# Optimization experiments

Measured on AMD Instinct MI355X. Metric: run time of the kernel, lower is better.

The kernel has to match this reference:

```python
import jax, jax.numpy as jnp
import numpy as np
import math

B, T, C = 2, 2048, 2048
N_HEAD = 16
N_KV = 4
GROUP = N_HEAD // N_KV
HS = C // N_HEAD
WINDOW = 1024
SINK = 4


def setup_inputs() -> dict:
    key = jax.random.key(0)
    ks = jax.random.split(key, 5)
    s = 1.0 / math.sqrt(C)
    return {
        "x": jax.random.normal(ks[0], (B, T, C), dtype=jnp.float32),
        "Wq": jax.random.normal(ks[1], (C, C), dtype=jnp.float32) * s,
        "Wk": jax.random.normal(ks[2], (N_KV * HS, C), dtype=jnp.float32) * s,
        "Wv": jax.random.normal(ks[3], (N_KV * HS, C), dtype=jnp.float32) * s,
        "Wo": jax.random.normal(ks[4], (C, C), dtype=jnp.float32) * s,
    }


def _sliding_window_sink_mask(t):
    i = jnp.arange(t)[:, None]  # query index
    j = jnp.arange(t)[None, :]  # key index
    causal = j <= i
    band = j >= i - (WINDOW - 1)
    mask = causal & band
    mask = mask | (j < SINK)          # sink columns always visible
    mask = mask & ((i >= SINK) | causal)  # sink rows stay strictly causal
    return mask  # (T, T) bool


def reference(x, Wq, Wk, Wv, Wo):
    b, t, c = x.shape
    q = (x @ Wq.T).reshape(b, t, N_HEAD, HS).transpose(0, 2, 1, 3)
    # group q heads by kv head: (B, n_kv, group, T, hs)
    q = q.reshape(b, N_KV, GROUP, t, HS)
    k = (x @ Wk.T).reshape(b, t, N_KV, HS).transpose(0, 2, 1, 3)  # (B, n_kv, T, hs)
    v = (x @ Wv.T).reshape(b, t, N_KV, HS).transpose(0, 2, 1, 3)
    scale = 1.0 / math.sqrt(HS)
    # scores over full TxT (faithful to original, K/V expansion done via broadcast)
    att = jnp.einsum('bkgqd,bkjd->bkgqj', q, k) * scale
    mask = _sliding_window_sink_mask(t)  # (T, T)
    att = jnp.where(mask[None, None, None, :, :], att, -jnp.inf)
    att = jax.nn.softmax(att, axis=-1)
    y = jnp.einsum('bkgqj,bkjd->bkgqd', att, v)
    y = y.reshape(b, N_HEAD, t, HS).transpose(0, 2, 1, 3).reshape(b, t, c)
    return y @ Wo.T
```

## Files before the change

### kernel.cpp

```cpp
#include <hip/hip_runtime.h>


#define T_SEQ 2048
#define NKV   4
#define HS    128
#define CDIM  2048
#define QKVN  3072
#define WIN   1024
#define SINKN 4

typedef __bf16 bf16x8 __attribute__((ext_vector_type(8)));
typedef float  f32x4  __attribute__((ext_vector_type(4)));

#define MFMA16(A, B, C) __builtin_amdgcn_mfma_f32_16x16x32_bf16(A, B, C, 0, 0, 0)
#define EXP2(x) __builtin_amdgcn_exp2f(x)

__device__ inline unsigned short f2bu(float f) {
  unsigned int u = __float_as_uint(f);
  u += 0x7fffu + ((u >> 16) & 1u);
  return (unsigned short)(u >> 16);
}
__device__ inline unsigned int pkhi(float f0, float f1) {
  return __builtin_amdgcn_perm(__float_as_uint(f1), __float_as_uint(f0),
                               0x07060302u);
}
__device__ inline __bf16 us2b(unsigned short u) {
  union { unsigned short u; __bf16 b; } t; t.u = u; return t.b;
}
__device__ inline f32x4 fzero4() { f32x4 z = {0.f, 0.f, 0.f, 0.f}; return z; }

__device__ __forceinline__ void glds16(const void* g, const void* lds_uniform) {
  typedef __attribute__((address_space(1))) void gv;
  typedef __attribute__((address_space(3))) void lv;
  __builtin_amdgcn_global_load_lds((gv*)(unsigned long long)g,
                                   (lv*)(unsigned int)(unsigned long long)lds_uniform,
                                   16, 0, 0);
}

#define SZ_X  8388608
#define SZ_WQ 4194304
#define SZ_WK 1048576
#define OFF_WQ (SZ_X)
#define OFF_WK (SZ_X + SZ_WQ)
#define OFF_WV (OFF_WK + SZ_WK)
#define OFF_WO (OFF_WV + SZ_WK)
#define SZ_ALL (OFF_WO + SZ_WQ)

__global__ __launch_bounds__(256) void f2b_all(const float* __restrict__ x,
                                               const float* __restrict__ wq,
                                               const float* __restrict__ wk,
                                               const float* __restrict__ wv,
                                               const float* __restrict__ wo,
                                               unsigned short* __restrict__ out,
                                               float qs) {
  int i = (blockIdx.x * 256 + threadIdx.x) * 4;
  const float* src; int off; float sc = 1.0f;
  if (i < OFF_WQ)      { src = x;  off = 0; }
  else if (i < OFF_WK) { src = wq; off = OFF_WQ; sc = qs; }
  else if (i < OFF_WV) { src = wk; off = OFF_WK; }
  else if (i < OFF_WO) { src = wv; off = OFF_WV; }
  else                 { src = wo; off = OFF_WO; }
  float4 v = *reinterpret_cast<const float4*>(src + (i - off));
  ushort4 o;
  o.x = f2bu(v.x * sc); o.y = f2bu(v.y * sc);
  o.z = f2bu(v.z * sc); o.w = f2bu(v.w * sc);
  *reinterpret_cast<ushort4*>(out + i) = o;
}

__device__ inline void storeC(unsigned short* p, float v) { *p = f2bu(v); }
__device__ inline void storeC(float* p, float v) { *p = v; }

template <typename OutT>
__global__ __launch_bounds__(512, 2) void gemm_bn192(const unsigned short* __restrict__ A,
                                                     const unsigned short* __restrict__ B,
                                                     OutT* __restrict__ C,
                                                     int M, int N, int K) {
  __shared__ __align__(16) unsigned short As[2][16384];
  __shared__ __align__(16) unsigned short Bs[2][12288];
  const int tid  = threadIdx.x;
  const int wave = tid >> 6, lane = tid & 63;
  const int quad = lane >> 4, l16 = lane & 15;
  const int wmi  = wave >> 1, wni = wave & 1;
  const int sx   = ((l16 >> 3) & 1) << 5;

  const int tmn  = M >> 8;
  const int qq   = gridDim.x >> 3;
  const int swzb = (blockIdx.x & 7) * qq + (blockIdx.x >> 3);
  const int tm   = (swzb % tmn) << 8;
  const int tn   = (swzb / tmn) * 192;

  const int logl = (lane * 16) ^ (((lane >> 5) & 1) << 5);
  const int srow = logl >> 6;
  const int scol = (logl & 63) >> 1;
  const int NT   = K >> 6;

  auto issueA = [&](int tt, int ch) {
    glds16(&A[(size_t)(tm + (ch & 15) * 16 + srow) * K + (tt << 6) + (ch >> 4) * 32 + scol],
           (const char*)As + ((tt & 1) << 15) + ch * 1024);
  };
  auto issueB = [&](int tt, int kh, int rb) {
    glds16(&B[(size_t)(tn + rb * 16 + srow) * K + (tt << 6) + kh * 32 + scol],
           (const char*)Bs + (tt & 1) * 24576 + (kh * 12 + rb) * 1024);
  };
  const int g3kh = (wave >= 4) ? 1 : 0;
  const int g3rb = (wave >= 4) ? (wave - 4) : (8 + wave);

  f32x4 acc[4][6];
#pragma unroll
  for (int i = 0; i < 4; ++i)
#pragma unroll
    for (int j = 0; j < 6; ++j) acc[i][j] = fzero4();

  issueA(0, wave); issueA(0, 8 + wave); issueB(0, 0, wave);
  issueA(0, 16 + wave); issueA(0, 24 + wave); issueB(0, 1, 4 + wave);
  issueB(0, g3kh, g3rb);
  if (NT > 1) {
    issueA(1, wave); issueA(1, 8 + wave); issueB(1, 0, wave);
    asm volatile("s_waitcnt vmcnt(3)" ::: "memory");
  } else {
    asm volatile("s_waitcnt vmcnt(0)" ::: "memory");
  }
  __builtin_amdgcn_s_barrier();

  for (int t = 0; t < NT; ++t) {
    const char* Asc = (const char*)As + ((t & 1) << 15);
    const char* Bsc = (const char*)Bs + (t & 1) * 24576;
    const bool h1 = (t + 1 < NT), h2 = (t + 2 < NT);
    bf16x8 aq[4], bq[6];

#pragma unroll
    for (int g = 0; g < 6; ++g)
      bq[g] = *reinterpret_cast<const bf16x8*>(
          Bsc + (((wni * 96 + g * 16 + l16) << 6) + ((quad * 16) ^ sx)));
#pragma unroll
    for (int f = 0; f < 4; ++f)
      aq[f] = *reinterpret_cast<const bf16x8*>(
          Asc + (((wmi * 64 + f * 16 + l16) << 6) + ((quad * 16) ^ sx)));
    if (h1) {
      issueA(t + 1, 16 + wave); issueA(t + 1, 24 + wave);
      issueB(t + 1, 1, 4 + wave); issueB(t + 1, g3kh, g3rb);
    }
    __builtin_amdgcn_s_barrier();
    asm volatile("s_waitcnt lgkmcnt(0)" ::: "memory");
    __builtin_amdgcn_s_setprio(1);
#pragma unroll
    for (int f = 0; f < 4; ++f)
#pragma unroll
      for (int g = 0; g < 6; ++g) acc[f][g] = MFMA16(aq[f], bq[g], acc[f][g]);
    __builtin_amdgcn_s_setprio(0);
    if (h1) asm volatile("s_waitcnt vmcnt(7)" ::: "memory");
    else    asm volatile("s_waitcnt vmcnt(0)" ::: "memory");
    __builtin_amdgcn_s_barrier();

#pragma unroll
    for (int g = 0; g < 6; ++g)
      bq[g] = *reinterpret_cast<const bf16x8*>(
          Bsc + (12288 + ((wni * 96 + g * 16 + l16) << 6) + ((quad * 16) ^ sx)));
#pragma unroll
    for (int f = 0; f < 4; ++f)
      aq[f] = *reinterpret_cast<const bf16x8*>(
          Asc + (16384 + ((wmi * 64 + f * 16 + l16) << 6) + ((quad * 16) ^ sx)));
    if (h2) {
      issueA(t + 2, wave); issueA(t + 2, 8 + wave); issueB(t + 2, 0, wave);
    }
    __builtin_amdgcn_s_barrier();
    asm volatile("s_waitcnt lgkmcnt(0)" ::: "memory");
    __builtin_amdgcn_s_setprio(1);
#pragma unroll
    for (int f = 0; f < 4; ++f)
#pragma unroll
      for (int g = 0; g < 6; ++g) acc[f][g] = MFMA16(aq[f], bq[g], acc[f][g]);
    __builtin_amdgcn_s_setprio(0);
    if (h2)      asm volatile("s_waitcnt vmcnt(7)" ::: "memory");
    else if (h1) asm volatile("s_waitcnt vmcnt(4)" ::: "memory");
    else         asm volatile("s_waitcnt vmcnt(0)" ::: "memory");
    __builtin_amdgcn_s_barrier();
  }

#pragma unroll
  for (int fi = 0; fi < 4; ++fi)
#pragma unroll
    for (int g = 0; g < 6; ++g)
#pragma unroll
      for (int r = 0; r < 4; ++r) {
        const int row = tm + wmi * 64 + fi * 16 + quad * 4 + r;
        const int col = tn + wni * 96 + g * 16 + l16;
        storeC(&C[(size_t)row * N + col], acc[fi][g][r]);
      }
}

template <typename OutT>
__global__ __launch_bounds__(512, 2) void gemm_bn128(const unsigned short* __restrict__ A,
                                                     const unsigned short* __restrict__ B,
                                                     OutT* __restrict__ C,
                                                     int M, int N, int K) {
  __shared__ __align__(16) unsigned short As[2][16384];
  __shared__ __align__(16) unsigned short Bs[2][8192];
  const int tid  = threadIdx.x;
  const int wave = tid >> 6, lane = tid & 63;
  const int quad = lane >> 4, l16 = lane & 15;
  const int wmi  = wave >> 1, wni = wave & 1;
  const int sx   = ((l16 >> 3) & 1) << 5;

  const int tmn  = M >> 8;
  const int qq   = gridDim.x >> 3;
  const int swzb = (blockIdx.x & 7) * qq + (blockIdx.x >> 3);
  const int tm   = (swzb % tmn) << 8;
  const int tn   = (swzb / tmn) << 7;

  const int logl = (lane * 16) ^ (((lane >> 5) & 1) << 5);
  const int srow = logl >> 6;
  const int scol = (logl & 63) >> 1;
  const int NT   = K >> 6;

  auto issueA = [&](int tt, int ch) {
    glds16(&A[(size_t)(tm + (ch & 15) * 16 + srow) * K + (tt << 6) + (ch >> 4) * 32 + scol],
           (const char*)As + ((tt & 1) << 15) + ch * 1024);
  };
  auto issueB = [&](int tt, int ch) {
    glds16(&B[(size_t)(tn + (ch & 7) * 16 + srow) * K + (tt << 6) + (ch >> 3) * 32 + scol],
           (const char*)Bs + ((tt & 1) << 14) + ch * 1024);
  };

  f32x4 acc[4][4];
#pragma unroll
  for (int i = 0; i < 4; ++i)
#pragma unroll
    for (int j = 0; j < 4; ++j) acc[i][j] = fzero4();

  issueB(0, wave);     issueA(0, wave);      issueA(0, 8 + wave);
  issueB(0, 8 + wave); issueA(0, 16 + wave); issueA(0, 24 + wave);
  if (NT > 1) {
    issueB(1, wave); issueA(1, wave); issueA(1, 8 + wave);
    asm volatile("s_waitcnt vmcnt(6)" ::: "memory");
  } else {
    asm volatile("s_waitcnt vmcnt(3)" ::: "memory");
  }
  __builtin_amdgcn_s_barrier();

  for (int t = 0; t < NT; ++t) {
    const char* Asc = (const char*)As + ((t & 1) << 15);
    const char* Bsc = (const char*)Bs + ((t & 1) << 14);
    const bool h1 = (t + 1 < NT), h2 = (t + 2 < NT);
    bf16x8 aq[4], bq[4];

#pragma unroll
    for (int g = 0; g < 4; ++g)
      bq[g] = *reinterpret_cast<const bf16x8*>(
          Bsc + (((wni * 64 + g * 16 + l16) << 6) + ((quad * 16) ^ sx)));
#pragma unroll
    for (int f = 0; f < 4; ++f)
      aq[f] = *reinterpret_cast<const bf16x8*>(
          Asc + (((wmi * 64 + f * 16 + l16) << 6) + ((quad * 16) ^ sx)));
    if (h1) {
      issueB(t + 1, 8 + wave); issueA(t + 1, 16 + wave); issueA(t + 1, 24 + wave);
    }
    __builtin_amdgcn_s_barrier();
    asm volatile("s_waitcnt lgkmcnt(0)" ::: "memory");
    __builtin_amdgcn_s_setprio(1);
#pragma unroll
    for (int f = 0; f < 4; ++f)
#pragma unroll
      for (int g = 0; g < 4; ++g) acc[f][g] = MFMA16(aq[f], bq[g], acc[f][g]);
    __builtin_amdgcn_s_setprio(0);
    if (h1) asm volatile("s_waitcnt vmcnt(6)" ::: "memory");
    else    asm volatile("s_waitcnt vmcnt(0)" ::: "memory");
    __builtin_amdgcn_s_barrier();

#pragma unroll
    for (int g = 0; g < 4; ++g)
      bq[g] = *reinterpret_cast<const bf16x8*>(
          Bsc + (8192 + ((wni * 64 + g * 16 + l16) << 6) + ((quad * 16) ^ sx)));
#pragma unroll
    for (int f = 0; f < 4; ++f)
      aq[f] = *reinterpret_cast<const bf16x8*>(
          Asc + (16384 + ((wmi * 64 + f * 16 + l16) << 6) + ((quad * 16) ^ sx)));
    if (h2) {
      issueB(t + 2, wave); issueA(t + 2, wave); issueA(t + 2, 8 + wave);
    }
    __builtin_amdgcn_s_barrier();
    asm volatile("s_waitcnt lgkmcnt(0)" ::: "memory");
    __builtin_amdgcn_s_setprio(1);
#pragma unroll
    for (int f = 0; f < 4; ++f)
#pragma unroll
      for (int g = 0; g < 4; ++g) acc[f][g] = MFMA16(aq[f], bq[g], acc[f][g]);
    __builtin_amdgcn_s_setprio(0);
    if (h2)      asm volatile("s_waitcnt vmcnt(6)" ::: "memory");
    else if (h1) asm volatile("s_waitcnt vmcnt(3)" ::: "memory");
    else         asm volatile("s_waitcnt vmcnt(0)" ::: "memory");
    __builtin_amdgcn_s_barrier();
  }

#pragma unroll
  for (int fi = 0; fi < 4; ++fi)
#pragma unroll
    for (int g = 0; g < 4; ++g)
#pragma unroll
      for (int r = 0; r < 4; ++r) {
        const int row = tm + wmi * 64 + fi * 16 + quad * 4 + r;
        const int col = tn + wni * 64 + g * 16 + l16;
        storeC(&C[(size_t)row * N + col], acc[fi][g][r]);
      }
}

__global__ __launch_bounds__(256) void kvpack(const unsigned short* __restrict__ QKV,
                                              unsigned short* __restrict__ Kp,
                                              unsigned short* __restrict__ Vp) {
  const int tid  = threadIdx.x;
  const int kt64 = blockIdx.x;
  const int bk   = blockIdx.y;
  const int b = bk >> 2, kvh = bk & 3;
  const int kt = kt64 * 64;
  const int bT = b * T_SEQ;
  const int dq = tid & 15;

  unsigned short* kdst = &Kp[(size_t)(bk * 32 + kt64) * 8192];
#pragma unroll
  for (int it = 0; it < 4; ++it) {
    int key = it * 16 + (tid >> 4);
    float4 v = *reinterpret_cast<const float4*>(
        &QKV[(size_t)(bT + kt + key) * QKVN + 2048 + kvh * HS + dq * 8]);
    int c = dq >> 2, quad = dq & 3, nt = key & 3, l16s = key >> 2;
    *reinterpret_cast<float4*>(
        &kdst[((size_t)((c * 4 + nt) * 64 + quad * 16 + l16s)) * 8]) = v;
  }

#pragma unroll
  for (int it = 0; it < 4; ++it) {
    int key = it * 16 + (tid >> 4);
    float4 v = *reinterpret_cast<const float4*>(
        &QKV[(size_t)(bT + kt + key) * QKVN + 2560 + kvh * HS + dq * 8]);
    const unsigned short* pv = reinterpret_cast<const unsigned short*>(&v);
    int kt32 = kt64 * 2 + (key >> 5);
    int quad = (key & 31) >> 3, j = key & 7;
    unsigned short* vdst = &Vp[(size_t)(bk * 64 + kt32) * 4096];
#pragma unroll
    for (int j2 = 0; j2 < 8; ++j2) {
      int d = dq * 8 + j2, dt = d >> 4, l16v = d & 15;
      vdst[((size_t)(dt * 64 + quad * 16 + l16v)) * 8 + j] = pv[j2];
    }
  }
}

__global__ __launch_bounds__(256) void attn_kernel(const unsigned short* __restrict__ QKV,
                                                   const unsigned short* __restrict__ Kp,
                                                   const unsigned short* __restrict__ Vp,
                                                   unsigned short* __restrict__ Y) {
  __shared__ __align__(16) unsigned short Ks[2][8192];
  __shared__ __align__(16) unsigned short Vs[2][8192];
  __shared__ __align__(16) unsigned short Ps[4 * 2048];

  const int tid  = threadIdx.x;
  const int wave = tid >> 6, lane = tid & 63;
  const int quad = lane >> 4, l16 = lane & 15;
  const int bk   = blockIdx.x & 7;
  const int seq  = blockIdx.x >> 3;
  const int qt0  = (63 - seq) * 32;
  const int kvh  = bk & 3, b = bk >> 2;
  const int h    = kvh * 4 + wave;
  const int bT   = b * T_SEQ;
  char* Pw = (char*)&Ps[wave * 2048];

  bf16x8 qa[2][4];
#pragma unroll
  for (int mt = 0; mt < 2; ++mt)
#pragma unroll
    for (int c = 0; c < 4; ++c)
      qa[mt][c] = *reinterpret_cast<const bf16x8*>(
          &QKV[(size_t)(bT + qt0 + mt * 16 + l16) * QKVN + h * HS + c * 32 + quad * 8]);

  bf16x8 ones;
#pragma unroll
  for (int j = 0; j < 8; ++j) ones[j] = us2b(0x3F80);

  f32x4 o[2][9];
#pragma unroll
  for (int mt = 0; mt < 2; ++mt)
#pragma unroll
    for (int dt = 0; dt < 9; ++dt) o[mt][dt] = fzero4();

  const int start = (qt0 >= 1024) ? ((qt0 - 1023) & ~63) : 0;
  const int sink  = (start > 0) ? 1 : 0;
  const int nch   = ((qt0 + 32 - start + 63) >> 6) + sink;

  auto stage = [&](int ci, int buf) {
    const int kt = (sink && ci == 0) ? 0 : start + (ci - sink) * 64;
    const unsigned short* kg = &Kp[(size_t)(bk * 32 + (kt >> 6)) * 8192 + lane * 8];
    const unsigned short* vg = &Vp[(size_t)(bk * 64 + (kt >> 5)) * 4096 + lane * 8];
#pragma unroll
    for (int i = 0; i < 4; ++i) {
      int part = wave * 4 + i;
      glds16(kg + part * 512, &Ks[buf][part * 512]);
      glds16(vg + part * 512, &Vs[buf][part * 512]);
    }
  };

  stage(0, 0);

  for (int ci = 0; ci < nch; ++ci) {
    const int  buf = ci & 1;
    const bool is_sink = (sink && ci == 0);
    const int  kt  = is_sink ? 0 : start + (ci - sink) * 64;
    const int  rem = qt0 + 32 - kt;
    const int  kcmax = is_sink ? 1 : (rem >= 64 ? 2 : ((rem + 31) >> 5));
    const bool full  = !is_sink && (kt + 63 <= qt0) && (kt >= qt0 - 992);

    if (ci + 1 < nch) {
      stage(ci + 1, buf ^ 1);
      asm volatile("s_waitcnt vmcnt(8)" ::: "memory");
    } else {
      asm volatile("s_waitcnt vmcnt(0)" ::: "memory");
    }
    __builtin_amdgcn_s_barrier();

    f32x4 s[2][4];
#pragma unroll
    for (int nt = 0; nt < 4; ++nt) { s[0][nt] = fzero4(); s[1][nt] = fzero4(); }
    __builtin_amdgcn_s_setprio(1);
#pragma unroll
    for (int c = 0; c < 4; ++c) {
#pragma unroll
      for (int nt = 0; nt < 4; ++nt) {
        bf16x8 kf = *reinterpret_cast<const bf16x8*>(&Ks[buf][(c * 4 + nt) * 512 + lane * 8]);
        s[0][nt] = MFMA16(qa[0][c], kf, s[0][nt]);
        s[1][nt] = MFMA16(qa[1][c], kf, s[1][nt]);
      }
    }
    __builtin_amdgcn_s_setprio(0);

    if (full) {
#pragma unroll
      for (int mt = 0; mt < 2; ++mt)
#pragma unroll
        for (int r = 0; r < 4; ++r) {
          const int row = mt * 16 + quad * 4 + r;
          uint2 pk;
          pk.x = pkhi(EXP2(s[mt][0][r]), EXP2(s[mt][1][r]));
          pk.y = pkhi(EXP2(s[mt][2][r]), EXP2(s[mt][3][r]));
          *reinterpret_cast<uint2*>(
              Pw + ((row * 128 + l16 * 8) ^ ((row & 7) << 4))) = pk;
        }
    } else {
#pragma unroll
      for (int mt = 0; mt < 2; ++mt)
#pragma unroll
        for (int r = 0; r < 4; ++r) {
          const int row = mt * 16 + quad * 4 + r;
          const int qi  = qt0 + row;
          float p[4];
#pragma unroll
          for (int nt = 0; nt < 4; ++nt) {
            int kj = kt + l16 * 4 + nt;
            bool ok = ((kj <= qi) && (kj + (WIN - 1) >= qi)) ||
                      ((kj < SINKN) && (qi >= SINKN));
            p[nt] = ok ? EXP2(s[mt][nt][r]) : 0.f;
          }
          uint2 pk;
          pk.x = pkhi(p[0], p[1]);
          pk.y = pkhi(p[2], p[3]);
          *reinterpret_cast<uint2*>(
              Pw + ((row * 128 + l16 * 8) ^ ((row & 7) << 4))) = pk;
        }
    }
    asm volatile("s_waitcnt lgkmcnt(0)" ::: "memory");

    __builtin_amdgcn_s_setprio(1);
#pragma unroll
    for (int kc = 0; kc < 2; ++kc)
      if (kc < kcmax) {
#pragma unroll
        for (int mt = 0; mt < 2; ++mt) {
          const int prow = mt * 16 + l16;
          bf16x8 pf = *reinterpret_cast<const bf16x8*>(
              Pw + ((prow * 128 + kc * 64 + quad * 16) ^ ((prow & 7) << 4)));
#pragma unroll
          for (int dt = 0; dt < 8; ++dt) {
            bf16x8 vf = *reinterpret_cast<const bf16x8*>(
                &Vs[buf][kc * 4096 + dt * 512 + lane * 8]);
            o[mt][dt] = MFMA16(pf, vf, o[mt][dt]);
          }
          o[mt][8] = MFMA16(pf, ones, o[mt][8]);
        }
      }
    __builtin_amdgcn_s_setprio(0);
    asm volatile("" ::: "memory");
    __builtin_amdgcn_s_barrier();
  }

  __syncthreads();
  unsigned short* Yst = &Ks[0][0];
#pragma unroll
  for (int mt = 0; mt < 2; ++mt) {
    float inv[4];
#pragma unroll
    for (int r = 0; r < 4; ++r) inv[r] = __builtin_amdgcn_rcpf(o[mt][8][r]);
#pragma unroll
    for (int dt = 0; dt < 8; ++dt)
#pragma unroll
      for (int r = 0; r < 4; ++r)
        Yst[(mt * 16 + quad * 4 + r) * 512 + wave * 128 + dt * 16 + l16] =
            f2bu(o[mt][dt][r] * inv[r]);
  }
  __syncthreads();
#pragma unroll
  for (int it = 0; it < 8; ++it) {
    int idx = it * 256 + tid;
    int row = idx >> 6, col = (idx & 63) * 8;
    *reinterpret_cast<uint4*>(
        &Y[(size_t)(bT + qt0 + row) * CDIM + kvh * 512 + col]) =
        *reinterpret_cast<const uint4*>(&Yst[row * 512 + col]);
  }
}

extern "C" void kernel_launch(void* const* d_in, const int* in_sizes, int n_in,
                              void* d_out, int out_size, void* d_ws, size_t ws_size,
                              hipStream_t stream) {
  const float* x  = (const float*)d_in[0];
  const float* Wq = (const float*)d_in[1];
  const float* Wk = (const float*)d_in[2];
  const float* Wv = (const float*)d_in[3];
  const float* Wo = (const float*)d_in[4];
  float* out = (float*)d_out;

  unsigned short* base = (unsigned short*)d_ws;
  unsigned short* xb   = base;
  unsigned short* wqb  = xb + OFF_WQ;
  unsigned short* wob  = xb + OFF_WO;
  unsigned short* QKVb = xb + SZ_ALL;
  unsigned short* Kpb  = wqb;
  unsigned short* Vpb  = wqb + 2097152;
  unsigned short* Yb   = xb;

  const float qscale = 0.08838834764831845f * 1.4426950408889634f;
  f2b_all<<<SZ_ALL / 1024, 256, 0, stream>>>(x, Wq, Wk, Wv, Wo, xb, qscale);

  gemm_bn192<unsigned short><<<256, 512, 0, stream>>>(xb, wqb, QKVb, 4096, QKVN, 2048);

  kvpack<<<dim3(32, 8), 256, 0, stream>>>(QKVb, Kpb, Vpb);

  attn_kernel<<<512, 256, 0, stream>>>(QKVb, Kpb, Vpb, Yb);

  gemm_bn128<float><<<256, 512, 0, stream>>>(Yb, wob, out, 4096, 2048, 2048);
}
```

Before: 249.0 us.

## Split attention key chunk across wave pairs and double grid size

Each block now handles 2 query heads instead of 4. Every pair of waves splits the 64-key chunk into two 32-key halves, each wave computing scores and PV for its half. Partial outputs and row sums are then reduced through shared memory at the end. The grid doubles to 1024 blocks for more parallelism and less per-wave serial work, but each block re-stages the same K/V tiles for fewer heads, so K/V traffic doubles. The K pack layout is changed to match the new score column mapping.

Result: slower. 259.9 us (+4.4%).

```diff
diff --git a/kernel.cpp b/kernel.cpp
--- a/kernel.cpp
+++ b/kernel.cpp
@@ -20,9 +20,8 @@
   u += 0x7fffu + ((u >> 16) & 1u);
   return (unsigned short)(u >> 16);
 }
-__device__ inline unsigned int pkhi(float f0, float f1) {
-  return __builtin_amdgcn_perm(__float_as_uint(f1), __float_as_uint(f0),
-                               0x07060302u);
+__device__ inline unsigned short hi16(float f) {
+  return (unsigned short)(__float_as_uint(f) >> 16);
 }
 __device__ inline __bf16 us2b(unsigned short u) {
   union { unsigned short u; __bf16 b; } t; t.u = u; return t.b;
@@ -321,7 +320,7 @@
     int key = it * 16 + (tid >> 4);
     float4 v = *reinterpret_cast<const float4*>(
         &QKV[(size_t)(bT + kt + key) * QKVN + 2048 + kvh * HS + dq * 8]);
-    int c = dq >> 2, quad = dq & 3, nt = key & 3, l16s = key >> 2;
+    int c = dq >> 2, quad = dq & 3, nt = key >> 4, l16s = key & 15;
     *reinterpret_cast<float4*>(
         &kdst[((size_t)((c * 4 + nt) * 64 + quad * 16 + l16s)) * 8]) = v;
   }
@@ -349,18 +348,21 @@
                                                    unsigned short* __restrict__ Y) {
   __shared__ __align__(16) unsigned short Ks[2][8192];
   __shared__ __align__(16) unsigned short Vs[2][8192];
-  __shared__ __align__(16) unsigned short Ps[4 * 2048];
+  __shared__ __align__(16) unsigned short Ps[2][2048];
 
   const int tid  = threadIdx.x;
   const int wave = tid >> 6, lane = tid & 63;
   const int quad = lane >> 4, l16 = lane & 15;
+  const int hh   = wave >> 1, kcw = wave & 1;
   const int bk   = blockIdx.x & 7;
-  const int seq  = blockIdx.x >> 3;
+  const int idx2 = blockIdx.x >> 3;
+  const int hp   = idx2 & 1;
+  const int seq  = idx2 >> 1;
   const int qt0  = (63 - seq) * 32;
   const int kvh  = bk & 3, b = bk >> 2;
-  const int h    = kvh * 4 + wave;
+  const int h    = kvh * 4 + hp * 2 + hh;
   const int bT   = b * T_SEQ;
-  char* Pw = (char*)&Ps[wave * 2048];
+  char* Pw = (char*)&Ps[hh][0];
 
   bf16x8 qa[2][4];
 #pragma unroll
@@ -414,102 +416,129 @@
     }
     __builtin_amdgcn_s_barrier();
 
-    f32x4 s[2][4];
-#pragma unroll
-    for (int nt = 0; nt < 4; ++nt) { s[0][nt] = fzero4(); s[1][nt] = fzero4(); }
-    __builtin_amdgcn_s_setprio(1);
-#pragma unroll
-    for (int c = 0; c < 4; ++c) {
-#pragma unroll
-      for (int nt = 0; nt < 4; ++nt) {
-        bf16x8 kf = *reinterpret_cast<const bf16x8*>(&Ks[buf][(c * 4 + nt) * 512 + lane * 8]);
-        s[0][nt] = MFMA16(qa[0][c], kf, s[0][nt]);
-        s[1][nt] = MFMA16(qa[1][c], kf, s[1][nt]);
-      }
-    }
-    __builtin_amdgcn_s_setprio(0);
-
-    if (full) {
+    if (kcw < kcmax) {
+      f32x4 s[2][2];
+      s[0][0] = fzero4(); s[0][1] = fzero4();
+      s[1][0] = fzero4(); s[1][1] = fzero4();
+      __builtin_amdgcn_s_setprio(1);
+#pragma unroll
+      for (int c = 0; c < 4; ++c) {
+#pragma unroll
+        for (int ntp = 0; ntp < 2; ++ntp) {
+          bf16x8 kf = *reinterpret_cast<const bf16x8*>(
+              &Ks[buf][(c * 4 + 2 * kcw + ntp) * 512 + lane * 8]);
+          s[0][ntp] = MFMA16(qa[0][c], kf, s[0][ntp]);
+          s[1][ntp] = MFMA16(qa[1][c], kf, s[1][ntp]);
+        }
+      }
+      __builtin_amdgcn_s_setprio(0);
+
+      if (full) {
+#pragma unroll
+        for (int mt = 0; mt < 2; ++mt)
+#pragma unroll
+          for (int r = 0; r < 4; ++r) {
+            const int row = mt * 16 + quad * 4 + r;
+            const int swz = (row & 7) << 4;
+#pragma unroll
+            for (int ntp = 0; ntp < 2; ++ntp) {
+              int e2 = (2 * kcw + ntp) * 32 + l16 * 2;
+              *reinterpret_cast<unsigned short*>(Pw + ((row * 128 + e2) ^ swz)) =
+                  hi16(EXP2(s[mt][ntp][r]));
+            }
+          }
+      } else {
+#pragma unroll
+        for (int mt = 0; mt < 2; ++mt)
+#pragma unroll
+          for (int r = 0; r < 4; ++r) {
+            const int row = mt * 16 + quad * 4 + r;
+            const int qi  = qt0 + row;
+            const int swz = (row & 7) << 4;
+#pragma unroll
+            for (int ntp = 0; ntp < 2; ++ntp) {
+              int kj = kt + (2 * kcw + ntp) * 16 + l16;
+              bool ok = ((kj <= qi) && (kj + (WIN - 1) >= qi)) ||
+                        ((kj < SINKN) && (qi >= SINKN));
+              float p = ok ? EXP2(s[mt][ntp][r]) : 0.f;
+              int e2 = (2 * kcw + ntp) * 32 + l16 * 2;
+              *reinterpret_cast<unsigned short*>(Pw + ((row * 128 + e2) ^ swz)) =
+                  hi16(p);
+            }
+          }
+      }
+      asm volatile("s_waitcnt lgkmcnt(0)" ::: "memory");
+
+      __builtin_amdgcn_s_setprio(1);
+      bf16x8 pf[2];
+#pragma unroll
+      for (int mt = 0; mt < 2; ++mt) {
+        const int prow = mt * 16 + l16;
+        pf[mt] = *reinterpret_cast<const bf16x8*>(
+            Pw + ((prow * 128 + kcw * 64 + quad * 16) ^ ((prow & 7) << 4)));
+      }
+#pragma unroll
+      for (int dt = 0; dt < 8; ++dt) {
+        bf16x8 vf = *reinterpret_cast<const bf16x8*>(
+            &Vs[buf][kcw * 4096 + dt * 512 + lane * 8]);
+        o[0][dt] = MFMA16(pf[0], vf, o[0][dt]);
+        o[1][dt] = MFMA16(pf[1], vf, o[1][dt]);
+      }
+      o[0][8] = MFMA16(pf[0], ones, o[0][8]);
+      o[1][8] = MFMA16(pf[1], ones, o[1][8]);
+      __builtin_amdgcn_s_setprio(0);
+    }
+    asm volatile("" ::: "memory");
+    __builtin_amdgcn_s_barrier();
+  }
+
+  __syncthreads();
+  {
+    char* scr = (hh == 0) ? (char*)&Ks[0][0] : (char*)&Vs[0][0];
+    if (kcw == 1) {
 #pragma unroll
       for (int mt = 0; mt < 2; ++mt)
 #pragma unroll
-        for (int r = 0; r < 4; ++r) {
-          const int row = mt * 16 + quad * 4 + r;
-          uint2 pk;
-          pk.x = pkhi(EXP2(s[mt][0][r]), EXP2(s[mt][1][r]));
-          pk.y = pkhi(EXP2(s[mt][2][r]), EXP2(s[mt][3][r]));
-          *reinterpret_cast<uint2*>(
-              Pw + ((row * 128 + l16 * 8) ^ ((row & 7) << 4))) = pk;
+        for (int dt = 0; dt < 9; ++dt)
+          *reinterpret_cast<f32x4*>(scr + ((mt * 9 + dt) * 64 + lane) * 16) =
+              o[mt][dt];
+    }
+    __syncthreads();
+    if (kcw == 0) {
+      char* yst = scr + 20480;
+#pragma unroll
+      for (int mt = 0; mt < 2; ++mt) {
+#pragma unroll
+        for (int dt = 0; dt < 9; ++dt) {
+          f32x4 part = *reinterpret_cast<const f32x4*>(
+              scr + ((mt * 9 + dt) * 64 + lane) * 16);
+#pragma unroll
+          for (int r = 0; r < 4; ++r) o[mt][dt][r] += part[r];
         }
-    } else {
-#pragma unroll
-      for (int mt = 0; mt < 2; ++mt)
-#pragma unroll
-        for (int r = 0; r < 4; ++r) {
-          const int row = mt * 16 + quad * 4 + r;
-          const int qi  = qt0 + row;
-          float p[4];
-#pragma unroll
-          for (int nt = 0; nt < 4; ++nt) {
-            int kj = kt + l16 * 4 + nt;
-            bool ok = ((kj <= qi) && (kj + (WIN - 1) >= qi)) ||
-                      ((kj < SINKN) && (qi >= SINKN));
-            p[nt] = ok ? EXP2(s[mt][nt][r]) : 0.f;
-          }
-          uint2 pk;
-          pk.x = pkhi(p[0], p[1]);
-          pk.y = pkhi(p[2], p[3]);
-          *reinterpret_cast<uint2*>(
-              Pw + ((row * 128 + l16 * 8) ^ ((row & 7) << 4))) = pk;
-        }
-    }
-    asm volatile("s_waitcnt lgkmcnt(0)" ::: "memory");
-
-    __builtin_amdgcn_s_setprio(1);
-#pragma unroll
-    for (int kc = 0; kc < 2; ++kc)
-      if (kc < kcmax) {
-#pragma unroll
-        for (int mt = 0; mt < 2; ++mt) {
-          const int prow = mt * 16 + l16;
-          bf16x8 pf = *reinterpret_cast<const bf16x8*>(
-              Pw + ((prow * 128 + kc * 64 + quad * 16) ^ ((prow & 7) << 4)));
-#pragma unroll
-          for (int dt = 0; dt < 8; ++dt) {
-            bf16x8 vf = *reinterpret_cast<const bf16x8*>(
-                &Vs[buf][kc * 4096 + dt * 512 + lane * 8]);
-            o[mt][dt] = MFMA16(pf, vf, o[mt][dt]);
-          }
-          o[mt][8] = MFMA16(pf, ones, o[mt][8]);
-        }
-      }
-    __builtin_amdgcn_s_setprio(0);
-    asm volatile("" ::: "memory");
-    __builtin_amdgcn_s_barrier();
-  }
-
+        float inv[4];
+#pragma unroll
+        for (int r = 0; r < 4; ++r) inv[r] = __builtin_amdgcn_rcpf(o[mt][8][r]);
+#pragma unroll
+        for (int dt = 0; dt < 8; ++dt)
+#pragma unroll
+          for (int r = 0; r < 4; ++r)
+            *reinterpret_cast<unsigned short*>(
+                yst + ((mt * 16 + quad * 4 + r) * 128 + dt * 16 + l16) * 2) =
+                f2bu(o[mt][dt][r] * inv[r]);
+      }
+    }
+  }
   __syncthreads();
-  unsigned short* Yst = &Ks[0][0];
-#pragma unroll
-  for (int mt = 0; mt < 2; ++mt) {
-    float inv[4];
-#pragma unroll
-    for (int r = 0; r < 4; ++r) inv[r] = __builtin_amdgcn_rcpf(o[mt][8][r]);
-#pragma unroll
-    for (int dt = 0; dt < 8; ++dt)
-#pragma unroll
-      for (int r = 0; r < 4; ++r)
-        Yst[(mt * 16 + quad * 4 + r) * 512 + wave * 128 + dt * 16 + l16] =
-            f2bu(o[mt][dt][r] * inv[r]);
-  }
-  __syncthreads();
-#pragma unroll
-  for (int it = 0; it < 8; ++it) {
+#pragma unroll
+  for (int it = 0; it < 4; ++it) {
     int idx = it * 256 + tid;
-    int row = idx >> 6, col = (idx & 63) * 8;
+    int hh2 = idx >> 9, rem2 = idx & 511;
+    int row = rem2 >> 4, colc = (rem2 & 15) * 8;
+    const char* src = ((hh2 == 0) ? (const char*)&Ks[0][0] : (const char*)&Vs[0][0]) +
+                      20480 + (row * 128 + colc) * 2;
     *reinterpret_cast<uint4*>(
-        &Y[(size_t)(bT + qt0 + row) * CDIM + kvh * 512 + col]) =
-        *reinterpret_cast<const uint4*>(&Yst[row * 512 + col]);
+        &Y[(size_t)(bT + qt0 + row) * CDIM + kvh * 512 + hp * 256 + hh2 * 128 + colc]) =
+        *reinterpret_cast<const uint4*>(src);
   }
 }
 
@@ -539,7 +568,7 @@
 
   kvpack<<<dim3(32, 8), 256, 0, stream>>>(QKVb, Kpb, Vpb);
 
-  attn_kernel<<<512, 256, 0, stream>>>(QKVb, Kpb, Vpb, Yb);
+  attn_kernel<<<1024, 256, 0, stream>>>(QKVb, Kpb, Vpb, Yb);
 
   gemm_bn128<float><<<256, 512, 0, stream>>>(Yb, wob, out, 4096, 2048, 2048);
 }
```
